# Kernel tuning notes

Measured on AMD Instinct MI355X. Metric: run time of the kernel, lower is better.

## Reference

```python
import jax, jax.numpy as jnp
import numpy as np

B, C, H, W = 8, 256, 56, 56
K = 3  # kernel size


def _unfold3x3(x):
    """torch nn.Unfold(kernel=3, stride=1, pad=1) -> [B, HW, C*9].

    torch orders the unfolded channel dim as (c, ki, kj) with c slowest.
    """
    b, c, h, w = x.shape
    xp = jnp.pad(x, ((0, 0), (0, 0), (1, 1), (1, 1)))
    # stack 9 shifted views -> [B, C, 9, H, W]
    patches = jnp.stack(
        [xp[:, :, i:i + h, j:j + w] for i in range(K) for j in range(K)],
        axis=2,
    )
    return patches.reshape(b, c * K * K, h * w).transpose(0, 2, 1)


def setup_inputs() -> dict:
    key = jax.random.key(0)
    ks = jax.random.split(key, 8)
    d = C * K * K  # 2304
    s1 = 1.0 / np.sqrt(d)
    s2 = 1.0 / np.sqrt(C)
    return {
        "x": jax.random.normal(ks[0], (B, C, H, W), jnp.float32),
        "W1": jax.random.uniform(ks[1], (d, C), jnp.float32, -s1, s1),
        "b1": jax.random.uniform(ks[2], (C,), jnp.float32, -s1, s1),
        "W2": jax.random.uniform(ks[3], (C, d), jnp.float32, -s2, s2),
        "b2": jax.random.uniform(ks[4], (d,), jnp.float32, -s2, s2),
        "W3": jax.random.uniform(ks[5], (d, C), jnp.float32, -s1, s1),
        "b3": jax.random.uniform(ks[6], (C,), jnp.float32, -s1, s1),
    }


def reference(x, W1, b1, W2, b2, W3, b3):
    t = _unfold3x3(x)                                   # [B, HW, C*9]
    h1 = jax.nn.relu(jnp.einsum('bld,dc->blc', t, W1) + b1)   # [B, HW, C]
    s = jax.nn.sigmoid(jnp.einsum('blc,cd->bld', h1, W2) + b2)  # [B, HW, C*9]
    out = jnp.einsum('bld,dc->blc', t * s, W3) + b3     # [B, HW, C]
    return out
```

## Files before the change

### kernel.cpp

```cpp
#include <hip/hip_runtime.h>

typedef unsigned short u16;
typedef unsigned int u32;
typedef __attribute__((ext_vector_type(8))) short bfrag_t;
typedef __attribute__((ext_vector_type(4))) float accfrag_t;
typedef __attribute__((ext_vector_type(4))) u32 u32x4;

__device__ __forceinline__ u16 f2b(float f) {
    u32 u = __float_as_uint(f);
    u32 r = (u + 0x7FFFu + ((u >> 16) & 1u)) >> 16;
    return (u16)r;
}
__device__ __forceinline__ u32 pkbf16(float lo, float hi) {
    u32 r;
    asm("v_cvt_pk_bf16_f32 %0, %1, %2" : "=v"(r) : "v"(lo), "v"(hi));
    return r;
}
__device__ __forceinline__ float blo(u32 v) { return __uint_as_float(v << 16); }
__device__ __forceinline__ float bhi(u32 v) { return __uint_as_float(v & 0xffff0000u); }

__device__ __forceinline__ void load16(const u16* g, u16* l) {
    __builtin_amdgcn_global_load_lds(
        (__attribute__((address_space(1))) void*)(u16*)g,
        (__attribute__((address_space(3))) void*)l,
        16, 0, 0);
}

__global__ __launch_bounds__(256) void k_prep(
    const float* __restrict__ x, const float* __restrict__ W1,
    const float* __restrict__ W2, const float* __restrict__ W3,
    const float* __restrict__ b2, u16* __restrict__ xtp,
    u16* __restrict__ W1f, u16* __restrict__ W2f,
    u16* __restrict__ W3f, float* __restrict__ b2p) {
    __shared__ __align__(16) char smem[29184];
    const int bid = blockIdx.x;
    const int tid = threadIdx.x;
    if (bid < 928) {
        const int b = bid / 116;
        const int r = bid - b * 116;
        const int hp = r >> 1;
        const int ch = r & 1;
        u16* rowbase = xtp + (size_t)(b * 58 + hp) * 58 * 256;
        if (hp == 0 || hp == 57) {
            if (ch == 0) {
                u32* p = (u32*)rowbase;
                for (int i = tid; i < 58 * 128; i += 256) p[i] = 0;
            }
            return;
        }
        float* lds = (float*)smem;
        const int h = hp - 1;
        const int c0 = ch * 128;
        const float* xb = x + (size_t)(b * 256 + c0) * 3136 + h * 56;
#pragma unroll
        for (int it = 0; it < 7; ++it) {
            const int idx = it * 256 + tid;
            const int cl = idx / 14;
            const int f4 = idx - cl * 14;
            const float4 v = *(const float4*)(xb + (size_t)cl * 3136 + f4 * 4);
            float* d = lds + cl * 57 + f4 * 4;
            d[0] = v.x; d[1] = v.y; d[2] = v.z; d[3] = v.w;
        }
        __syncthreads();
        u32* orow = (u32*)rowbase;
        const int cp = tid & 63;
        const int wg = tid >> 6;
        const float* l0p = lds + (2 * cp) * 57;
        const float* l1p = lds + (2 * cp + 1) * 57;
#pragma unroll
        for (int it = 0; it < 15; ++it) {
            const int wp = it * 4 + wg;
            if (wp < 58) {
                u32 val = 0;
                if (wp >= 1 && wp <= 56) val = pkbf16(l0p[wp - 1], l1p[wp - 1]);
                orow[wp * 128 + ch * 64 + cp] = val;
            }
        }
    } else if (bid < 1072) {
        int b = bid - 928;
        const float* in = b < 72 ? W1 : W3;
        u16* out = b < 72 ? W1f : W3f;
        if (b >= 72) b -= 72;
        const int rrp = b >> 3;
        const int cg = b & 7;
        u16* lds1 = (u16*)smem;
#pragma unroll
        for (int cc = 0; cc < 32; ++cc) {
            int d = (cg * 32 + cc) * 9 + rrp;
            lds1[cc * 256 + tid] = f2b(in[d * 256 + tid]);
        }
        __syncthreads();
        const int kc72 = rrp * 8 + cg;
#pragma unroll
        for (int s = 0; s < 32; ++s) {
            const int w = s >> 2;
            const int o = (s & 3) * 256 + tid;
            const int e = o & 7;
            const int ln = (o >> 3) & 63;
            const int j = o >> 9;
            const int n = w * 32 + j * 16 + (ln & 15);
            const int q = (ln >> 4) * 8 + e;
            out[(w * 72 + kc72) * 1024 + o] = lds1[q * 256 + n];
        }
    } else if (bid < 1144) {
        const int b = bid - 1072;
        const int rr = b >> 3;
        const int w = b & 7;
        u16* lds2 = (u16*)smem;
#pragma unroll
        for (int s = 0; s < 32; ++s) {
            int li = s * 256 + tid;
            int k = li >> 5, dloc = li & 31;
            lds2[k * 32 + dloc] = f2b(W2[k * 2304 + (w * 32 + dloc) * 9 + rr]);
        }
        __syncthreads();
        u16* ob = W2f + (rr * 8 + w) * 8192;
#pragma unroll
        for (int s = 0; s < 32; ++s) {
            const int o = s * 256 + tid;
            const int e = o & 7;
            const int ln = (o >> 3) & 63;
            const int j = (o >> 9) & 1;
            const int kc = o >> 10;
            const int k = kc * 32 + (ln >> 4) * 8 + e;
            const int dloc = j * 16 + (ln & 15);
            ob[o] = lds2[k * 32 + dloc];
        }
    } else {
        int idx = (bid - 1144) * 256 + tid;
        if (idx < 2304) b2p[idx] = b2[(idx & 255) * 9 + (idx >> 8)];
    }
}

__global__ __launch_bounds__(512, 4) void k_fused(
    const u16* __restrict__ xtp, const u16* __restrict__ W1f,
    const u16* __restrict__ W2f, const u16* __restrict__ W3f,
    const float* __restrict__ b1, const float* __restrict__ b2p,
    const float* __restrict__ b3, float* __restrict__ out) {
    __shared__ __align__(16) u16 As[16384];
    __shared__ __align__(16) u16 Us[16384];

    const int tid = threadIdx.x;
    const int wave = tid >> 6;
    const int lane = tid & 63;
    const int fr = lane & 15;
    const int fq = lane >> 4;
    const int l0 = blockIdx.x * 64;
    const int hi = tid >> 8;

    int roff;
    {
        int l = l0 + ((tid >> 2) & 63);
        int b = l / 3136;
        int rem = l - b * 3136;
        int h = rem / 56;
        int w = rem - h * 56;
        roff = ((b * 58 + h + 1) * 58 + (w + 1)) * 256 +
               (((tid & 3) ^ ((tid >> 3) & 3)) * 8);
    }
    const int stageOff = (wave & 3) * 512 + lane * 8;
    const int aoff = fr * 32 + ((fq ^ ((fr >> 1) & 3)) * 8);
    auto shiftOf = [](int rr) { return ((rr / 3 - 1) * 58 + (rr % 3) - 1) * 256; };
    auto stage = [&](u16* buf, int shift) {
#pragma unroll
        for (int q = 0; q < 4; ++q) {
            const int kc = 2 * q + hi;
            load16(xtp + roff + shift + kc * 32, buf + kc * 2048 + stageOff);
        }
    };
    auto ewidx = [&](int i, int j, int r) {
        const int row = i * 16 + fq * 4 + r;
        const int sl = (j * 2 + (fr >> 3)) ^ ((fq * 2 + (r >> 1)) & 3);
        return row * 32 + sl * 8 + (fr & 7);
    };

    accfrag_t acc[4][2], accO[4][2];
#pragma unroll
    for (int i = 0; i < 4; ++i)
#pragma unroll
        for (int j = 0; j < 2; ++j) {
            acc[i][j] = (accfrag_t)0.f;
            accO[i][j] = (accfrag_t)0.f;
        }

    const u16* w1p = W1f + wave * 73728 + lane * 8;
    stage(As, shiftOf(0));
    for (int rr = 0; rr < 9; ++rr) {
        u16* cur = (rr & 1) ? Us : As;
        u16* nxt = (rr & 1) ? As : Us;
        __syncthreads();
        if (rr < 8) stage(nxt, shiftOf(rr + 1));
#pragma unroll
        for (int kc = 0; kc < 8; ++kc) {
            bfrag_t bf[2], af[4];
#pragma unroll
            for (int j = 0; j < 2; ++j)
                bf[j] = *(const bfrag_t*)(w1p + ((rr * 8 + kc) * 2 + j) * 512);
#pragma unroll
            for (int i = 0; i < 4; ++i)
                af[i] = *(const bfrag_t*)(cur + kc * 2048 + i * 512 + aoff);
#pragma unroll
            for (int i = 0; i < 4; ++i)
#pragma unroll
                for (int j = 0; j < 2; ++j)
                    acc[i][j] = __builtin_amdgcn_mfma_f32_16x16x32_bf16(
                        af[i], bf[j], acc[i][j], 0, 0, 0);
        }
    }
    __syncthreads();
#pragma unroll
    for (int i = 0; i < 4; ++i) {
#pragma unroll
        for (int j = 0; j < 2; ++j) {
            const float bv = b1[wave * 32 + j * 16 + fr];
#pragma unroll
            for (int r = 0; r < 4; ++r) {
                float v = acc[i][j][r] + bv;
                v = v > 0.f ? v : 0.f;
                const float vh = __shfl_down(v, 1);
                if (!(lane & 1))
                    *(u32*)&As[wave * 2048 + ewidx(i, j, r)] = pkbf16(v, vh);
            }
        }
    }
    __syncthreads();

    const u16* w3p = W3f + wave * 73728 + lane * 8;
    for (int rr = 0; rr < 9; ++rr) {
        const int shift = shiftOf(rr);
        u32x4 tvreg[4];
#pragma unroll
        for (int q = 0; q < 4; ++q) {
            const int kc = 2 * q + hi;
            tvreg[q] = *(const u32x4*)(xtp + roff + shift + kc * 32);
        }
#pragma unroll
        for (int i = 0; i < 4; ++i)
#pragma unroll
            for (int j = 0; j < 2; ++j) acc[i][j] = (accfrag_t)0.f;
        const u16* w2p = W2f + (rr * 8 + wave) * 8192 + lane * 8;
#pragma unroll
        for (int kc = 0; kc < 8; ++kc) {
            bfrag_t bf[2], af[4];
#pragma unroll
            for (int j = 0; j < 2; ++j)
                bf[j] = *(const bfrag_t*)(w2p + (kc * 2 + j) * 512);
#pragma unroll
            for (int i = 0; i < 4; ++i)
                af[i] = *(const bfrag_t*)(As + kc * 2048 + i * 512 + aoff);
#pragma unroll
            for (int i = 0; i < 4; ++i)
#pragma unroll
                for (int j = 0; j < 2; ++j)
                    acc[i][j] = __builtin_amdgcn_mfma_f32_16x16x32_bf16(
                        af[i], bf[j], acc[i][j], 0, 0, 0);
        }
        __syncthreads();
#pragma unroll
        for (int i = 0; i < 4; ++i) {
#pragma unroll
            for (int j = 0; j < 2; ++j) {
                const float bv = b2p[rr * 256 + wave * 32 + j * 16 + fr];
#pragma unroll
                for (int r = 0; r < 4; ++r) {
                    const float z = acc[i][j][r] + bv;
                    const float s = __builtin_amdgcn_rcpf(1.f + __expf(-z));
                    const float sh = __shfl_down(s, 1);
                    if (!(lane & 1))
                        *(u32*)&Us[wave * 2048 + ewidx(i, j, r)] = pkbf16(s, sh);
                }
            }
        }
        __syncthreads();
#pragma unroll
        for (int q = 0; q < 4; ++q) {
            const int kc = 2 * q + hi;
            const int idx = kc * 2048 + ((tid * 8) & 2047);
            u32x4 sv = *(const u32x4*)(Us + idx);
            u32x4 rv;
#pragma unroll
            for (int e = 0; e < 4; ++e)
                rv[e] = pkbf16(blo(sv[e]) * blo(tvreg[q][e]),
                               bhi(sv[e]) * bhi(tvreg[q][e]));
            *(u32x4*)(Us + idx) = rv;
        }
        __syncthreads();
#pragma unroll
        for (int kc = 0; kc < 8; ++kc) {
            bfrag_t bf[2], af[4];
#pragma unroll
            for (int j = 0; j < 2; ++j)
                bf[j] = *(const bfrag_t*)(w3p + ((rr * 8 + kc) * 2 + j) * 512);
#pragma unroll
            for (int i = 0; i < 4; ++i)
                af[i] = *(const bfrag_t*)(Us + kc * 2048 + i * 512 + aoff);
#pragma unroll
            for (int i = 0; i < 4; ++i)
#pragma unroll
                for (int j = 0; j < 2; ++j)
                    accO[i][j] = __builtin_amdgcn_mfma_f32_16x16x32_bf16(
                        af[i], bf[j], accO[i][j], 0, 0, 0);
        }
    }

#pragma unroll
    for (int i = 0; i < 4; ++i) {
#pragma unroll
        for (int j = 0; j < 2; ++j) {
            const int col = wave * 32 + j * 16 + fr;
            const float bv = b3[col];
#pragma unroll
            for (int r = 0; r < 4; ++r) {
                const float v = accO[i][j][r] + bv;
                const float vh = __shfl_down(v, 1);
                if (!(lane & 1)) {
                    float2 st = make_float2(v, vh);
                    *(float2*)(out + (size_t)(l0 + i * 16 + fq * 4 + r) * 256 + col) = st;
                }
            }
        }
    }
}

extern "C" void kernel_launch(void* const* d_in, const int* in_sizes, int n_in,
                              void* d_out, int out_size, void* d_ws, size_t ws_size,
                              hipStream_t stream) {
    const float* x  = (const float*)d_in[0];
    const float* W1 = (const float*)d_in[1];
    const float* b1 = (const float*)d_in[2];
    const float* W2 = (const float*)d_in[3];
    const float* b2 = (const float*)d_in[4];
    const float* W3 = (const float*)d_in[5];
    const float* b3 = (const float*)d_in[6];
    float* out = (float*)d_out;

    char* ws = (char*)d_ws;
    u16* xtp = (u16*)ws;  ws += (size_t)8 * 58 * 58 * 256 * 2;
    u16* W1f = (u16*)ws;  ws += (size_t)589824 * 2;
    u16* W2f = (u16*)ws;  ws += (size_t)589824 * 2;
    u16* W3f = (u16*)ws;  ws += (size_t)589824 * 2;
    float* b2p = (float*)ws;

    k_prep<<<1153, 256, 0, stream>>>(x, W1, W2, W3, b2, xtp, W1f, W2f, W3f, b2p);
    k_fused<<<392, 512, 0, stream>>>(xtp, W1f, W2f, W3f, b1, b2p, b3, out);
}
```

Before: 208.7 us.

## Enlarge fused block tile to 112 pixels (two image rows) and double-buffer weight fragments

Each block now processes 112 output pixels (two full image rows of one batch) instead of 64, so the grid drops from 392 to 224 blocks and every weight fragment loaded from global memory feeds 7 row tiles instead of 4. Staging addresses are recomputed per wave for 7 chunks, the weight B fragments are software-prefetched one k-step ahead, and one barrier before the sigmoid*x multiply is removed because each wave now touches only its own LDS region. This cuts weight traffic per output but raises LDS use and register pressure, reducing occupancy to 2 blocks per CU. With 224 blocks on a GPU with 256 CUs, some CUs will also sit idle.

```diff
diff --git a/kernel.cpp b/kernel.cpp
--- a/kernel.cpp
+++ b/kernel.cpp
@@ -132,41 +132,43 @@
     }
 }
 
-__global__ __launch_bounds__(512, 4) void k_fused(
+__global__ __launch_bounds__(512, 2) void k_fused(
     const u16* __restrict__ xtp, const u16* __restrict__ W1f,
     const u16* __restrict__ W2f, const u16* __restrict__ W3f,
     const float* __restrict__ b1, const float* __restrict__ b2p,
     const float* __restrict__ b3, float* __restrict__ out) {
-    __shared__ __align__(16) u16 As[16384];
-    __shared__ __align__(16) u16 Us[16384];
+    __shared__ __align__(16) u16 As[28672];
+    __shared__ __align__(16) u16 Us[28672];
 
     const int tid = threadIdx.x;
     const int wave = tid >> 6;
     const int lane = tid & 63;
     const int fr = lane & 15;
     const int fq = lane >> 4;
-    const int l0 = blockIdx.x * 64;
-    const int hi = tid >> 8;
-
-    int roff;
-    {
-        int l = l0 + ((tid >> 2) & 63);
-        int b = l / 3136;
-        int rem = l - b * 3136;
-        int h = rem / 56;
-        int w = rem - h * 56;
-        roff = ((b * 58 + h + 1) * 58 + (w + 1)) * 256 +
-               (((tid & 3) ^ ((tid >> 3) & 3)) * 8);
-    }
-    const int stageOff = (wave & 3) * 512 + lane * 8;
+
+    const int bid = blockIdx.x;
+    const int b = bid / 28;
+    const int h0 = (bid - b * 28) * 2;
+    const int l0 = bid * 112;
+
+    int roffs[7];
+#pragma unroll
+    for (int q = 0; q < 7; ++q) {
+        const int m = q * 64 + lane;
+        const int row = m >> 2;
+        const int c8 = m & 3;
+        const int dh = row / 56;
+        const int w = row - dh * 56;
+        const int swz = c8 ^ ((row >> 1) & 3);
+        roffs[q] = ((b * 58 + h0 + dh + 1) * 58 + (w + 1)) * 256 + wave * 32 + swz * 8;
+    }
     const int aoff = fr * 32 + ((fq ^ ((fr >> 1) & 3)) * 8);
     auto shiftOf = [](int rr) { return ((rr / 3 - 1) * 58 + (rr % 3) - 1) * 256; };
     auto stage = [&](u16* buf, int shift) {
-#pragma unroll
-        for (int q = 0; q < 4; ++q) {
-            const int kc = 2 * q + hi;
-            load16(xtp + roff + shift + kc * 32, buf + kc * 2048 + stageOff);
-        }
+        u16* dst = buf + wave * 3584 + lane * 8;
+#pragma unroll
+        for (int q = 0; q < 7; ++q)
+            load16(xtp + roffs[q] + shift, dst + q * 512);
     };
     auto ewidx = [&](int i, int j, int r) {
         const int row = i * 16 + fq * 4 + r;
@@ -174,9 +176,9 @@
         return row * 32 + sl * 8 + (fr & 7);
     };
 
-    accfrag_t acc[4][2], accO[4][2];
-#pragma unroll
-    for (int i = 0; i < 4; ++i)
+    accfrag_t acc[7][2], accO[7][2];
+#pragma unroll
+    for (int i = 0; i < 7; ++i)
 #pragma unroll
         for (int j = 0; j < 2; ++j) {
             acc[i][j] = (accfrag_t)0.f;
@@ -190,26 +192,33 @@
         u16* nxt = (rr & 1) ? As : Us;
         __syncthreads();
         if (rr < 8) stage(nxt, shiftOf(rr + 1));
+        bfrag_t bf[2][2];
+#pragma unroll
+        for (int j = 0; j < 2; ++j)
+            bf[0][j] = *(const bfrag_t*)(w1p + ((rr * 8 + 0) * 2 + j) * 512);
 #pragma unroll
         for (int kc = 0; kc < 8; ++kc) {
-            bfrag_t bf[2], af[4];
-#pragma unroll
-            for (int j = 0; j < 2; ++j)
-                bf[j] = *(const bfrag_t*)(w1p + ((rr * 8 + kc) * 2 + j) * 512);
-#pragma unroll
-            for (int i = 0; i < 4; ++i)
-                af[i] = *(const bfrag_t*)(cur + kc * 2048 + i * 512 + aoff);
-#pragma unroll
-            for (int i = 0; i < 4; ++i)
+            if (kc < 7) {
+#pragma unroll
+                for (int j = 0; j < 2; ++j)
+                    bf[(kc + 1) & 1][j] =
+                        *(const bfrag_t*)(w1p + ((rr * 8 + kc + 1) * 2 + j) * 512);
+            }
+            bfrag_t af[7];
+#pragma unroll
+            for (int i = 0; i < 7; ++i)
+                af[i] = *(const bfrag_t*)(cur + kc * 3584 + i * 512 + aoff);
+#pragma unroll
+            for (int i = 0; i < 7; ++i)
 #pragma unroll
                 for (int j = 0; j < 2; ++j)
                     acc[i][j] = __builtin_amdgcn_mfma_f32_16x16x32_bf16(
-                        af[i], bf[j], acc[i][j], 0, 0, 0);
+                        af[i], bf[kc & 1][j], acc[i][j], 0, 0, 0);
         }
     }
     __syncthreads();
 #pragma unroll
-    for (int i = 0; i < 4; ++i) {
+    for (int i = 0; i < 7; ++i) {
 #pragma unroll
         for (int j = 0; j < 2; ++j) {
             const float bv = b1[wave * 32 + j * 16 + fr];
@@ -219,7 +228,7 @@
                 v = v > 0.f ? v : 0.f;
                 const float vh = __shfl_down(v, 1);
                 if (!(lane & 1))
-                    *(u32*)&As[wave * 2048 + ewidx(i, j, r)] = pkbf16(v, vh);
+                    *(u32*)&As[wave * 3584 + ewidx(i, j, r)] = pkbf16(v, vh);
             }
         }
     }
@@ -228,36 +237,43 @@
     const u16* w3p = W3f + wave * 73728 + lane * 8;
     for (int rr = 0; rr < 9; ++rr) {
         const int shift = shiftOf(rr);
-        u32x4 tvreg[4];
-#pragma unroll
-        for (int q = 0; q < 4; ++q) {
-            const int kc = 2 * q + hi;
-            tvreg[q] = *(const u32x4*)(xtp + roff + shift + kc * 32);
-        }
-#pragma unroll
-        for (int i = 0; i < 4; ++i)
+        u32x4 tvreg[7];
+#pragma unroll
+        for (int q = 0; q < 7; ++q)
+            tvreg[q] = *(const u32x4*)(xtp + roffs[q] + shift);
+#pragma unroll
+        for (int i = 0; i < 7; ++i)
 #pragma unroll
             for (int j = 0; j < 2; ++j) acc[i][j] = (accfrag_t)0.f;
         const u16* w2p = W2f + (rr * 8 + wave) * 8192 + lane * 8;
-#pragma unroll
-        for (int kc = 0; kc < 8; ++kc) {
-            bfrag_t bf[2], af[4];
+        {
+            bfrag_t bf[2][2];
 #pragma unroll
             for (int j = 0; j < 2; ++j)
-                bf[j] = *(const bfrag_t*)(w2p + (kc * 2 + j) * 512);
-#pragma unroll
-            for (int i = 0; i < 4; ++i)
-                af[i] = *(const bfrag_t*)(As + kc * 2048 + i * 512 + aoff);
-#pragma unroll
-            for (int i = 0; i < 4; ++i)
-#pragma unroll
-                for (int j = 0; j < 2; ++j)
-                    acc[i][j] = __builtin_amdgcn_mfma_f32_16x16x32_bf16(
-                        af[i], bf[j], acc[i][j], 0, 0, 0);
-        }
-        __syncthreads();
-#pragma unroll
-        for (int i = 0; i < 4; ++i) {
+                bf[0][j] = *(const bfrag_t*)(w2p + (0 * 2 + j) * 512);
+#pragma unroll
+            for (int kc = 0; kc < 8; ++kc) {
+                if (kc < 7) {
+#pragma unroll
+                    for (int j = 0; j < 2; ++j)
+                        bf[(kc + 1) & 1][j] =
+                            *(const bfrag_t*)(w2p + ((kc + 1) * 2 + j) * 512);
+                }
+                bfrag_t af[7];
+#pragma unroll
+                for (int i = 0; i < 7; ++i)
+                    af[i] = *(const bfrag_t*)(As + kc * 3584 + i * 512 + aoff);
+#pragma unroll
+                for (int i = 0; i < 7; ++i)
+#pragma unroll
+                    for (int j = 0; j < 2; ++j)
+                        acc[i][j] = __builtin_amdgcn_mfma_f32_16x16x32_bf16(
+                            af[i], bf[kc & 1][j], acc[i][j], 0, 0, 0);
+            }
+        }
+        __syncthreads();
+#pragma unroll
+        for (int i = 0; i < 7; ++i) {
 #pragma unroll
             for (int j = 0; j < 2; ++j) {
                 const float bv = b2p[rr * 256 + wave * 32 + j * 16 + fr];
@@ -267,15 +283,13 @@
                     const float s = __builtin_amdgcn_rcpf(1.f + __expf(-z));
                     const float sh = __shfl_down(s, 1);
                     if (!(lane & 1))
-                        *(u32*)&Us[wave * 2048 + ewidx(i, j, r)] = pkbf16(s, sh);
+                        *(u32*)&Us[wave * 3584 + ewidx(i, j, r)] = pkbf16(s, sh);
                 }
             }
         }
-        __syncthreads();
-#pragma unroll
-        for (int q = 0; q < 4; ++q) {
-            const int kc = 2 * q + hi;
-            const int idx = kc * 2048 + ((tid * 8) & 2047);
+#pragma unroll
+        for (int q = 0; q < 7; ++q) {
+            const int idx = wave * 3584 + (q * 64 + lane) * 8;
             u32x4 sv = *(const u32x4*)(Us + idx);
             u32x4 rv;
 #pragma unroll
@@ -285,26 +299,35 @@
             *(u32x4*)(Us + idx) = rv;
         }
         __syncthreads();
-#pragma unroll
-        for (int kc = 0; kc < 8; ++kc) {
-            bfrag_t bf[2], af[4];
+        {
+            bfrag_t bf[2][2];
 #pragma unroll
             for (int j = 0; j < 2; ++j)
-                bf[j] = *(const bfrag_t*)(w3p + ((rr * 8 + kc) * 2 + j) * 512);
-#pragma unroll
-            for (int i = 0; i < 4; ++i)
-                af[i] = *(const bfrag_t*)(Us + kc * 2048 + i * 512 + aoff);
-#pragma unroll
-            for (int i = 0; i < 4; ++i)
-#pragma unroll
-                for (int j = 0; j < 2; ++j)
-                    accO[i][j] = __builtin_amdgcn_mfma_f32_16x16x32_bf16(
-                        af[i], bf[j], accO[i][j], 0, 0, 0);
-        }
-    }
-
-#pragma unroll
-    for (int i = 0; i < 4; ++i) {
+                bf[0][j] = *(const bfrag_t*)(w3p + ((rr * 8 + 0) * 2 + j) * 512);
+#pragma unroll
+            for (int kc = 0; kc < 8; ++kc) {
+                if (kc < 7) {
+#pragma unroll
+                    for (int j = 0; j < 2; ++j)
+                        bf[(kc + 1) & 1][j] =
+                            *(const bfrag_t*)(w3p + ((rr * 8 + kc + 1) * 2 + j) * 512);
+                }
+                bfrag_t af[7];
+#pragma unroll
+                for (int i = 0; i < 7; ++i)
+                    af[i] = *(const bfrag_t*)(Us + kc * 3584 + i * 512 + aoff);
+#pragma unroll
+                for (int i = 0; i < 7; ++i)
+#pragma unroll
+                    for (int j = 0; j < 2; ++j)
+                        accO[i][j] = __builtin_amdgcn_mfma_f32_16x16x32_bf16(
+                            af[i], bf[kc & 1][j], accO[i][j], 0, 0, 0);
+            }
+        }
+    }
+
+#pragma unroll
+    for (int i = 0; i < 7; ++i) {
 #pragma unroll
         for (int j = 0; j < 2; ++j) {
             const int col = wave * 32 + j * 16 + fr;
@@ -342,5 +365,5 @@
     float* b2p = (float*)ws;
 
     k_prep<<<1153, 256, 0, stream>>>(x, W1, W2, W3, b2, xtp, W1f, W2f, W3f, b2p);
-    k_fused<<<392, 512, 0, stream>>>(xtp, W1f, W2f, W3f, b1, b2p, b3, out);
-}
+    k_fused<<<224, 512, 0, stream>>>(xtp, W1f, W2f, W3f, b1, b2p, b3, out);
+}
```

New measurement: 230.4 us. 10.4% more time.

## Remap x staging per wave, defer W3 GEMM, drop barriers, add setprio

Applied to the files above, without the earlier changes.

The x-tile staging and multiply mapping is reassigned so each wave owns one 32-channel slice across all 64 rows. The multiply step then reads and writes only its own wave's slice of Us. That lets two __syncthreads per tap be removed, with the W3 GEMM for tap rr-1 moved to the start of tap rr ahead of the W2 GEMM. MFMA sections are wrapped in s_setprio(1) so they get issue priority over other waves. The risk is correctness of the reduced barrier set and higher register pressure from the four precomputed offsets.

```diff
diff --git a/kernel.cpp b/kernel.cpp
--- a/kernel.cpp
+++ b/kernel.cpp
@@ -146,27 +146,26 @@
     const int fr = lane & 15;
     const int fq = lane >> 4;
     const int l0 = blockIdx.x * 64;
-    const int hi = tid >> 8;
-
-    int roff;
-    {
-        int l = l0 + ((tid >> 2) & 63);
-        int b = l / 3136;
-        int rem = l - b * 3136;
-        int h = rem / 56;
-        int w = rem - h * 56;
-        roff = ((b * 58 + h + 1) * 58 + (w + 1)) * 256 +
-               (((tid & 3) ^ ((tid >> 3) & 3)) * 8);
-    }
-    const int stageOff = (wave & 3) * 512 + lane * 8;
+
+    const int swz = (lane & 3) ^ ((lane >> 3) & 3);
+    int roffs[4], ldst[4];
+#pragma unroll
+    for (int q = 0; q < 4; ++q) {
+        const int row = q * 16 + (lane >> 2);
+        const int l = l0 + row;
+        const int b = l / 3136;
+        const int rem = l - b * 3136;
+        const int h = rem / 56;
+        const int w = rem - h * 56;
+        roffs[q] = ((b * 58 + h + 1) * 58 + (w + 1)) * 256 + wave * 32 + swz * 8;
+        ldst[q] = wave * 2048 + (q * 64 + lane) * 8;
+    }
     const int aoff = fr * 32 + ((fq ^ ((fr >> 1) & 3)) * 8);
     auto shiftOf = [](int rr) { return ((rr / 3 - 1) * 58 + (rr % 3) - 1) * 256; };
     auto stage = [&](u16* buf, int shift) {
 #pragma unroll
-        for (int q = 0; q < 4; ++q) {
-            const int kc = 2 * q + hi;
-            load16(xtp + roff + shift + kc * 32, buf + kc * 2048 + stageOff);
-        }
+        for (int q = 0; q < 4; ++q)
+            load16(xtp + roffs[q] + shift, buf + ldst[q]);
     };
     auto ewidx = [&](int i, int j, int r) {
         const int row = i * 16 + fq * 4 + r;
@@ -190,6 +189,7 @@
         u16* nxt = (rr & 1) ? As : Us;
         __syncthreads();
         if (rr < 8) stage(nxt, shiftOf(rr + 1));
+        __builtin_amdgcn_s_setprio(1);
 #pragma unroll
         for (int kc = 0; kc < 8; ++kc) {
             bfrag_t bf[2], af[4];
@@ -206,6 +206,7 @@
                     acc[i][j] = __builtin_amdgcn_mfma_f32_16x16x32_bf16(
                         af[i], bf[j], acc[i][j], 0, 0, 0);
         }
+        __builtin_amdgcn_s_setprio(0);
     }
     __syncthreads();
 #pragma unroll
@@ -226,19 +227,37 @@
     __syncthreads();
 
     const u16* w3p = W3f + wave * 73728 + lane * 8;
+    const u16* w2base = W2f + (wave)*8192 + lane * 8;
     for (int rr = 0; rr < 9; ++rr) {
+        __builtin_amdgcn_s_setprio(1);
+        if (rr > 0) {
+#pragma unroll
+            for (int kc = 0; kc < 8; ++kc) {
+                bfrag_t bf[2], af[4];
+#pragma unroll
+                for (int j = 0; j < 2; ++j)
+                    bf[j] = *(const bfrag_t*)(w3p + (((rr - 1) * 8 + kc) * 2 + j) * 512);
+#pragma unroll
+                for (int i = 0; i < 4; ++i)
+                    af[i] = *(const bfrag_t*)(Us + kc * 2048 + i * 512 + aoff);
+#pragma unroll
+                for (int i = 0; i < 4; ++i)
+#pragma unroll
+                    for (int j = 0; j < 2; ++j)
+                        accO[i][j] = __builtin_amdgcn_mfma_f32_16x16x32_bf16(
+                            af[i], bf[j], accO[i][j], 0, 0, 0);
+            }
+        }
         const int shift = shiftOf(rr);
         u32x4 tvreg[4];
 #pragma unroll
-        for (int q = 0; q < 4; ++q) {
-            const int kc = 2 * q + hi;
-            tvreg[q] = *(const u32x4*)(xtp + roff + shift + kc * 32);
-        }
+        for (int q = 0; q < 4; ++q)
+            tvreg[q] = *(const u32x4*)(xtp + roffs[q] + shift);
 #pragma unroll
         for (int i = 0; i < 4; ++i)
 #pragma unroll
             for (int j = 0; j < 2; ++j) acc[i][j] = (accfrag_t)0.f;
-        const u16* w2p = W2f + (rr * 8 + wave) * 8192 + lane * 8;
+        const u16* w2p = w2base + rr * 8 * 8192;
 #pragma unroll
         for (int kc = 0; kc < 8; ++kc) {
             bfrag_t bf[2], af[4];
@@ -255,6 +274,7 @@
                     acc[i][j] = __builtin_amdgcn_mfma_f32_16x16x32_bf16(
                         af[i], bf[j], acc[i][j], 0, 0, 0);
         }
+        __builtin_amdgcn_s_setprio(0);
         __syncthreads();
 #pragma unroll
         for (int i = 0; i < 4; ++i) {
@@ -271,37 +291,36 @@
                 }
             }
         }
-        __syncthreads();
 #pragma unroll
         for (int q = 0; q < 4; ++q) {
-            const int kc = 2 * q + hi;
-            const int idx = kc * 2048 + ((tid * 8) & 2047);
-            u32x4 sv = *(const u32x4*)(Us + idx);
+            u32x4 sv = *(const u32x4*)(Us + ldst[q]);
             u32x4 rv;
 #pragma unroll
             for (int e = 0; e < 4; ++e)
                 rv[e] = pkbf16(blo(sv[e]) * blo(tvreg[q][e]),
                                bhi(sv[e]) * bhi(tvreg[q][e]));
-            *(u32x4*)(Us + idx) = rv;
-        }
-        __syncthreads();
-#pragma unroll
-        for (int kc = 0; kc < 8; ++kc) {
-            bfrag_t bf[2], af[4];
+            *(u32x4*)(Us + ldst[q]) = rv;
+        }
+        __syncthreads();
+    }
+    __builtin_amdgcn_s_setprio(1);
+#pragma unroll
+    for (int kc = 0; kc < 8; ++kc) {
+        bfrag_t bf[2], af[4];
+#pragma unroll
+        for (int j = 0; j < 2; ++j)
+            bf[j] = *(const bfrag_t*)(w3p + ((8 * 8 + kc) * 2 + j) * 512);
+#pragma unroll
+        for (int i = 0; i < 4; ++i)
+            af[i] = *(const bfrag_t*)(Us + kc * 2048 + i * 512 + aoff);
+#pragma unroll
+        for (int i = 0; i < 4; ++i)
 #pragma unroll
             for (int j = 0; j < 2; ++j)
-                bf[j] = *(const bfrag_t*)(w3p + ((rr * 8 + kc) * 2 + j) * 512);
-#pragma unroll
-            for (int i = 0; i < 4; ++i)
-                af[i] = *(const bfrag_t*)(Us + kc * 2048 + i * 512 + aoff);
-#pragma unroll
-            for (int i = 0; i < 4; ++i)
-#pragma unroll
-                for (int j = 0; j < 2; ++j)
-                    accO[i][j] = __builtin_amdgcn_mfma_f32_16x16x32_bf16(
-                        af[i], bf[j], accO[i][j], 0, 0, 0);
-        }
-    }
+                accO[i][j] = __builtin_amdgcn_mfma_f32_16x16x32_bf16(
+                    af[i], bf[j], accO[i][j], 0, 0, 0);
+    }
+    __builtin_amdgcn_s_setprio(0);
 
 #pragma unroll
     for (int i = 0; i < 4; ++i) {
```

Result: no change. 206.9 us (-0.8%).
